# Optimization experiments

Hardware: AMD Instinct MI355X
Metric: run time of the kernel (lower is better)

## Reference

```python
import jax, jax.numpy as jnp
import numpy as np

N_ITEMS = 512
TABLE_SAMPLES = 2048
FULL_SIZE = 32768
PADDED_SIZE = 65536
BATCH = 8
N_EVENTS = 64


def setup_inputs() -> dict:
    key = jax.random.key(0)
    k1, k2, k3 = jax.random.split(key, 3)
    selections = jax.random.normal(k1, (BATCH, N_EVENTS, N_ITEMS), dtype=jnp.float32)
    # Envelopes init: uniform(-1,1) * linspace(1,0)**uniform(50,100) per item
    base = jax.random.uniform(k2, (N_ITEMS, TABLE_SAMPLES), minval=-1.0, maxval=1.0)
    exps = jax.random.uniform(jax.random.fold_in(k2, 1), (N_ITEMS, 1), minval=50.0, maxval=100.0)
    ramp = jnp.linspace(1.0, 0.0, TABLE_SAMPLES)[None, :]
    items = (base * ramp ** exps).astype(jnp.float32)
    # postprocess multiplies by uniform(-0.02, 0.02) noise of the interpolated shape
    noise = jax.random.uniform(k3, (BATCH, N_EVENTS, FULL_SIZE), minval=-0.02, maxval=0.02, dtype=jnp.float32)
    return {"selections": selections, "items": items, "noise": noise}


def reference(selections, items, noise):
    # preprocess_items: shift/scale into [0, ~1]
    items = items - items.min()
    items = items / (items.max() + 0.001)

    # select_items(..., type='sparse_softmax'): softmax over items, keep only
    # the max entry (scaled one-hot), then weighted combine against the table.
    sm = jax.nn.softmax(selections, axis=-1)                      # [b, e, n]
    w = jnp.max(sm, axis=-1, keepdims=True)                       # [b, e, 1]
    hard = jax.nn.one_hot(jnp.argmax(sm, axis=-1), sm.shape[-1], dtype=sm.dtype)
    sel = hard * w                                                # sparse one-hot weights
    selected = jnp.einsum('ben,nt->bet', sel, items)              # [b, e, T]

    # interpolate_last_axis: linear interpolation (half-pixel centers) to FULL_SIZE
    in_size = selected.shape[-1]
    pos = (jnp.arange(FULL_SIZE, dtype=jnp.float32) + 0.5) * (in_size / FULL_SIZE) - 0.5
    pos = jnp.clip(pos, 0.0, in_size - 1)
    lo = jnp.floor(pos).astype(jnp.int32)
    hi = jnp.minimum(lo + 1, in_size - 1)
    frac = (pos - lo).astype(selected.dtype)
    amp = selected[..., lo] * (1.0 - frac) + selected[..., hi] * frac  # [b, e, FULL]

    # multiply by noise, pad to PADDED_SIZE
    amp = amp * noise
    pad = jnp.zeros(amp.shape[:-1] + (PADDED_SIZE - FULL_SIZE,), dtype=amp.dtype)
    return jnp.concatenate([amp, pad], axis=-1)                   # [b, e, PADDED]
```

## Files before the change

kernel.cpp:

```cpp
#include <hip/hip_runtime.h>
#include <math.h>

constexpr int N_ITEMS = 512;
constexpr int TS      = 2048;
constexpr int FULL    = 32768;
constexpr int PADDED  = 65536;
constexpr int NPAIR   = 512;
constexpr int SPLIT   = 4;

using f4 = __attribute__((ext_vector_type(4))) float;

__device__ __forceinline__ unsigned fenc(float f) {
    unsigned u = __float_as_uint(f);
    return (u & 0x80000000u) ? ~u : (u | 0x80000000u);
}
__device__ __forceinline__ float fdec(unsigned e) {
    return __uint_as_float((e & 0x80000000u) ? (e & 0x7FFFFFFFu) : ~e);
}


__global__ void __launch_bounds__(256) k_prep(const f4* __restrict__ items4,
                                              const float* __restrict__ sel,
                                              unsigned* __restrict__ ws_min,
                                              unsigned* __restrict__ ws_max,
                                              int* __restrict__ ws_idx,
                                              float* __restrict__ ws_w) {
    __shared__ unsigned smin[4], smax[4];
    int blk = blockIdx.x;
    int tid = threadIdx.x;

    if (blk < 256) {
        unsigned lmin = 0xFFFFFFFFu, lmax = 0u;
        const int NV = (N_ITEMS * TS) / 4;
        for (int i = blk * 256 + tid; i < NV; i += 256 * 256) {
            f4 v = items4[i];
            unsigned e0 = fenc(v.x), e1 = fenc(v.y), e2 = fenc(v.z), e3 = fenc(v.w);
            lmin = min(min(min(lmin, e0), min(e1, e2)), e3);
            lmax = max(max(max(lmax, e0), max(e1, e2)), e3);
        }
        for (int off = 32; off > 0; off >>= 1) {
            lmin = min(lmin, (unsigned)__shfl_xor((int)lmin, off));
            lmax = max(lmax, (unsigned)__shfl_xor((int)lmax, off));
        }
        int wave = tid >> 6;
        if ((tid & 63) == 0) { smin[wave] = lmin; smax[wave] = lmax; }
        __syncthreads();
        if (tid == 0) {
            ws_min[blk] = min(min(smin[0], smin[1]), min(smin[2], smin[3]));
            ws_max[blk] = max(max(smax[0], smax[1]), max(smax[2], smax[3]));
        }
    } else {
        int p    = (blk - 256) * 4 + (tid >> 6);
        int lane = tid & 63;
        const float* s = sel + (size_t)p * N_ITEMS;
        float x[8];
        float vmax = -INFINITY;
        int   imax = 0x7FFFFFFF;
        #pragma unroll
        for (int k = 0; k < 8; ++k) {
            int i = lane + k * 64;
            x[k] = s[i];
            if (x[k] > vmax) { vmax = x[k]; imax = i; }
        }
        for (int off = 32; off > 0; off >>= 1) {
            float ov = __shfl_xor(vmax, off);
            int   oi = __shfl_xor(imax, off);
            if (ov > vmax || (ov == vmax && oi < imax)) { vmax = ov; imax = oi; }
        }
        float se = 0.0f;
        #pragma unroll
        for (int k = 0; k < 8; ++k) se += expf(x[k] - vmax);
        for (int off = 32; off > 0; off >>= 1) se += __shfl_xor(se, off);
        if (lane == 0) { ws_idx[p] = imax; ws_w[p] = 1.0f / se; }
    }
}

__global__ void __launch_bounds__(256, 8) k_main(const float* __restrict__ items,
                                                 const float* __restrict__ noise,
                                                 const unsigned* __restrict__ ws_min,
                                                 const unsigned* __restrict__ ws_max,
                                                 const int* __restrict__ ws_idx,
                                                 const float* __restrict__ ws_w,
                                                 float* __restrict__ out) {
    __shared__ float row[TS];

    int blk  = blockIdx.x;
    int p    = blk >> 2;
    int q    = blk & 3;
    int tid  = threadIdx.x;
    int lane = tid & 63;

    uint4 a = ((const uint4*)ws_min)[lane];
    uint4 c = ((const uint4*)ws_max)[lane];
    unsigned gmin = min(min(a.x, a.y), min(a.z, a.w));
    unsigned gmax = max(max(c.x, c.y), max(c.z, c.w));
    for (int off = 32; off > 0; off >>= 1) {
        gmin = min(gmin, (unsigned)__shfl_xor((int)gmin, off));
        gmax = max(gmax, (unsigned)__shfl_xor((int)gmax, off));
    }
    float minv  = fdec(gmin);
    float maxv  = fdec(gmax);
    float denom = (maxv - minv) + 0.001f;
    int   idx   = ws_idx[p];
    float scale = ws_w[p] / denom;
    float bias  = -minv * scale;

    constexpr int CHUNK  = FULL / SPLIT;
    constexpr int PCHUNK = (PADDED - FULL) / SPLIT;
    const f4* nz4  = (const f4*)(noise + (size_t)p * FULL + (size_t)q * CHUNK);
    f4*       o4   = (f4*)(out + (size_t)p * PADDED + (size_t)q * CHUNK);
    f4*       pad4 = (f4*)(out + (size_t)p * PADDED + FULL + (size_t)q * PCHUNK);
    int tbase = q * CHUNK;

    f4 nzv[8];
    #pragma unroll
    for (int k = 0; k < 8; ++k)
        nzv[k] = nz4[tid + k * 256];

    f4 z = {0.f, 0.f, 0.f, 0.f};
    #pragma unroll
    for (int k = 0; k < 8; ++k)
        pad4[tid + k * 256] = z;

    {
        const f4* it4 = (const f4*)(items + (size_t)idx * TS);
        f4 r0 = it4[tid];
        f4 r1 = it4[tid + 256];
        row[tid * 4 + 0] = fmaf(r0.x, scale, bias);
        row[tid * 4 + 1] = fmaf(r0.y, scale, bias);
        row[tid * 4 + 2] = fmaf(r0.z, scale, bias);
        row[tid * 4 + 3] = fmaf(r0.w, scale, bias);
        row[(tid + 256) * 4 + 0] = fmaf(r1.x, scale, bias);
        row[(tid + 256) * 4 + 1] = fmaf(r1.y, scale, bias);
        row[(tid + 256) * 4 + 2] = fmaf(r1.z, scale, bias);
        row[(tid + 256) * 4 + 3] = fmaf(r1.w, scale, bias);
    }
    __syncthreads();

    #pragma unroll
    for (int k = 0; k < 8; ++k) {
        int v  = tid + k * 256;
        int t0 = tbase + v * 4;
        float pos0 = ((float)t0 + 0.5f) * 0.0625f - 0.5f;
        f4 o;
        #pragma unroll
        for (int j = 0; j < 4; ++j) {
            float pj = fminf(fmaxf(pos0 + (float)j * 0.0625f, 0.0f), (float)(TS - 1));
            int   lj = (int)pj;
            int   hj = min(lj + 1, TS - 1);
            float fr = pj - (float)lj;
            float amp = row[lj] * (1.0f - fr) + row[hj] * fr;
            o[j] = amp * nzv[k][j];
        }
        o4[v] = o;
    }
}

extern "C" void kernel_launch(void* const* d_in, const int* in_sizes, int n_in,
                              void* d_out, int out_size, void* d_ws, size_t ws_size,
                              hipStream_t stream) {
    const float* sel   = (const float*)d_in[0];
    const float* items = (const float*)d_in[1];
    const float* noise = (const float*)d_in[2];
    float* out = (float*)d_out;

    unsigned* ws_min = (unsigned*)d_ws;
    unsigned* ws_max = (unsigned*)((char*)d_ws + 1024);
    int*      ws_idx = (int*)((char*)d_ws + 2048);
    float*    ws_w   = (float*)((char*)d_ws + 4096);

    hipLaunchKernelGGL(k_prep, dim3(384), dim3(256), 0, stream,
                       (const f4*)items, sel, ws_min, ws_max, ws_idx, ws_w);
    hipLaunchKernelGGL(k_main, dim3(NPAIR * SPLIT), dim3(256), 0, stream,
                       items, noise, ws_min, ws_max, ws_idx, ws_w, out);
}
```

Before: 39.62 us.

## Fuse prep and main kernels with atomic global min/max and spin-wait barrier

Merges the two-kernel pipeline into one launch. The first 256 blocks reduce the items min/max and publish the result through global atomics and a counter. Every block computes its own softmax argmax/weight, writes its padding and loads its rows, then spin-waits on the counter, with a timeout fallback that does a full local reduction. The affine normalization moves into the interpolation FMA and outputs use nontemporal stores. This removes one launch and the inter-kernel gap, but adds a memset launch, a cross-block spin dependency that relies on producer blocks being resident, and redundant per-block softmax work.

```diff
diff --git a/kernel.cpp b/kernel.cpp
--- a/kernel.cpp
+++ b/kernel.cpp
@@ -7,6 +7,8 @@
 constexpr int PADDED  = 65536;
 constexpr int NPAIR   = 512;
 constexpr int SPLIT   = 4;
+constexpr int NBLK    = NPAIR * SPLIT;
+constexpr int NPROD   = 256;
 
 using f4 = __attribute__((ext_vector_type(4))) float;
 
@@ -19,39 +21,48 @@
 }
 
 
-__global__ void __launch_bounds__(256) k_prep(const f4* __restrict__ items4,
-                                              const float* __restrict__ sel,
-                                              unsigned* __restrict__ ws_min,
-                                              unsigned* __restrict__ ws_max,
-                                              int* __restrict__ ws_idx,
-                                              float* __restrict__ ws_w) {
-    __shared__ unsigned smin[4], smax[4];
-    int blk = blockIdx.x;
-    int tid = threadIdx.x;
+__global__ void __launch_bounds__(256, 8) k_fused(const float* __restrict__ items,
+                                                  const float* __restrict__ sel,
+                                                  const float* __restrict__ noise,
+                                                  unsigned* __restrict__ ws,
+                                                  float* __restrict__ out) {
+    __shared__ float row[TS];
+    __shared__ unsigned sred[8];
+    __shared__ int s_idx;
+    __shared__ float s_w;
+    __shared__ int s_fb;
 
-    if (blk < 256) {
+    int b = blockIdx.x, t = threadIdx.x;
+    int lane = t & 63, wave = t >> 6;
+    int p = b >> 2, q = b & 3;
+
+    if (b < NPROD) {
+        const f4* it4 = (const f4*)items;
         unsigned lmin = 0xFFFFFFFFu, lmax = 0u;
-        const int NV = (N_ITEMS * TS) / 4;
-        for (int i = blk * 256 + tid; i < NV; i += 256 * 256) {
-            f4 v = items4[i];
+        #pragma unroll
+        for (int k = 0; k < 4; ++k) {
+            f4 v = it4[(size_t)k * 65536 + b * 256 + t];
             unsigned e0 = fenc(v.x), e1 = fenc(v.y), e2 = fenc(v.z), e3 = fenc(v.w);
-            lmin = min(min(min(lmin, e0), min(e1, e2)), e3);
-            lmax = max(max(max(lmax, e0), max(e1, e2)), e3);
+            lmin = min(lmin, min(min(e0, e1), min(e2, e3)));
+            lmax = max(lmax, max(max(e0, e1), max(e2, e3)));
         }
         for (int off = 32; off > 0; off >>= 1) {
             lmin = min(lmin, (unsigned)__shfl_xor((int)lmin, off));
             lmax = max(lmax, (unsigned)__shfl_xor((int)lmax, off));
         }
-        int wave = tid >> 6;
-        if ((tid & 63) == 0) { smin[wave] = lmin; smax[wave] = lmax; }
+        if (lane == 0) { sred[wave] = lmin; sred[4 + wave] = lmax; }
         __syncthreads();
-        if (tid == 0) {
-            ws_min[blk] = min(min(smin[0], smin[1]), min(smin[2], smin[3]));
-            ws_max[blk] = max(max(smax[0], smax[1]), max(smax[2], smax[3]));
+        if (t == 0) {
+            unsigned bmin = min(min(sred[0], sred[1]), min(sred[2], sred[3]));
+            unsigned bmax = max(max(sred[4], sred[5]), max(sred[6], sred[7]));
+            atomicMax(&ws[0], ~bmin);
+            atomicMax(&ws[1], bmax);
+            __threadfence();
+            atomicAdd(&ws[2], 1u);
         }
-    } else {
-        int p    = (blk - 256) * 4 + (tid >> 6);
-        int lane = tid & 63;
+    }
+
+    if (wave == 0) {
         const float* s = sel + (size_t)p * N_ITEMS;
         float x[8];
         float vmax = -INFINITY;
@@ -71,75 +82,82 @@
         #pragma unroll
         for (int k = 0; k < 8; ++k) se += expf(x[k] - vmax);
         for (int off = 32; off > 0; off >>= 1) se += __shfl_xor(se, off);
-        if (lane == 0) { ws_idx[p] = imax; ws_w[p] = 1.0f / se; }
+        if (lane == 0) { s_idx = imax; s_w = 1.0f / se; }
     }
-}
 
-__global__ void __launch_bounds__(256, 8) k_main(const float* __restrict__ items,
-                                                 const float* __restrict__ noise,
-                                                 const unsigned* __restrict__ ws_min,
-                                                 const unsigned* __restrict__ ws_max,
-                                                 const int* __restrict__ ws_idx,
-                                                 const float* __restrict__ ws_w,
-                                                 float* __restrict__ out) {
-    __shared__ float row[TS];
+    {
+        constexpr int PCHUNK = (PADDED - FULL) / SPLIT;
+        f4* pad4 = (f4*)(out + (size_t)p * PADDED + FULL + (size_t)q * PCHUNK);
+        f4 z = {0.f, 0.f, 0.f, 0.f};
+        #pragma unroll
+        for (int k = 0; k < 8; ++k)
+            __builtin_nontemporal_store(z, &pad4[t + k * 256]);
+    }
 
-    int blk  = blockIdx.x;
-    int p    = blk >> 2;
-    int q    = blk & 3;
-    int tid  = threadIdx.x;
-    int lane = tid & 63;
+    __syncthreads();
+    int   idx = s_idx;
+    float w   = s_w;
 
-    uint4 a = ((const uint4*)ws_min)[lane];
-    uint4 c = ((const uint4*)ws_max)[lane];
-    unsigned gmin = min(min(a.x, a.y), min(a.z, a.w));
-    unsigned gmax = max(max(c.x, c.y), max(c.z, c.w));
-    for (int off = 32; off > 0; off >>= 1) {
-        gmin = min(gmin, (unsigned)__shfl_xor((int)gmin, off));
-        gmax = max(gmax, (unsigned)__shfl_xor((int)gmax, off));
-    }
-    float minv  = fdec(gmin);
-    float maxv  = fdec(gmax);
-    float denom = (maxv - minv) + 0.001f;
-    int   idx   = ws_idx[p];
-    float scale = ws_w[p] / denom;
-    float bias  = -minv * scale;
+    const f4* it4 = (const f4*)(items + (size_t)idx * TS);
+    f4 r0 = it4[t];
+    f4 r1 = it4[t + 256];
 
-    constexpr int CHUNK  = FULL / SPLIT;
-    constexpr int PCHUNK = (PADDED - FULL) / SPLIT;
-    const f4* nz4  = (const f4*)(noise + (size_t)p * FULL + (size_t)q * CHUNK);
-    f4*       o4   = (f4*)(out + (size_t)p * PADDED + (size_t)q * CHUNK);
-    f4*       pad4 = (f4*)(out + (size_t)p * PADDED + FULL + (size_t)q * PCHUNK);
-    int tbase = q * CHUNK;
-
+    const f4* nz4 = (const f4*)(noise + (size_t)p * FULL + (size_t)q * (FULL / SPLIT));
     f4 nzv[8];
     #pragma unroll
     for (int k = 0; k < 8; ++k)
-        nzv[k] = nz4[tid + k * 256];
+        nzv[k] = nz4[t + k * 256];
 
-    f4 z = {0.f, 0.f, 0.f, 0.f};
-    #pragma unroll
-    for (int k = 0; k < 8; ++k)
-        pad4[tid + k * 256] = z;
+    ((f4*)row)[t]       = r0;
+    ((f4*)row)[t + 256] = r1;
 
-    {
-        const f4* it4 = (const f4*)(items + (size_t)idx * TS);
-        f4 r0 = it4[tid];
-        f4 r1 = it4[tid + 256];
-        row[tid * 4 + 0] = fmaf(r0.x, scale, bias);
-        row[tid * 4 + 1] = fmaf(r0.y, scale, bias);
-        row[tid * 4 + 2] = fmaf(r0.z, scale, bias);
-        row[tid * 4 + 3] = fmaf(r0.w, scale, bias);
-        row[(tid + 256) * 4 + 0] = fmaf(r1.x, scale, bias);
-        row[(tid + 256) * 4 + 1] = fmaf(r1.y, scale, bias);
-        row[(tid + 256) * 4 + 2] = fmaf(r1.z, scale, bias);
-        row[(tid + 256) * 4 + 3] = fmaf(r1.w, scale, bias);
+    if (t == 0) {
+        int fb = 0;
+        long long start = clock64();
+        while (__hip_atomic_load(&ws[2], __ATOMIC_ACQUIRE, __HIP_MEMORY_SCOPE_AGENT) < NPROD) {
+            __builtin_amdgcn_s_sleep(8);
+            if (clock64() - start > 10000000LL) { fb = 1; break; }
+        }
+        s_fb = fb;
     }
     __syncthreads();
 
+    float minv, maxv;
+    if (s_fb) {
+        const f4* a4 = (const f4*)items;
+        unsigned lmin = 0xFFFFFFFFu, lmax = 0u;
+        for (int i = t; i < (N_ITEMS * TS) / 4; i += 256) {
+            f4 v = a4[i];
+            unsigned e0 = fenc(v.x), e1 = fenc(v.y), e2 = fenc(v.z), e3 = fenc(v.w);
+            lmin = min(lmin, min(min(e0, e1), min(e2, e3)));
+            lmax = max(lmax, max(max(e0, e1), max(e2, e3)));
+        }
+        for (int off = 32; off > 0; off >>= 1) {
+            lmin = min(lmin, (unsigned)__shfl_xor((int)lmin, off));
+            lmax = max(lmax, (unsigned)__shfl_xor((int)lmax, off));
+        }
+        if (lane == 0) { sred[wave] = lmin; sred[4 + wave] = lmax; }
+        __syncthreads();
+        unsigned bmin = min(min(sred[0], sred[1]), min(sred[2], sred[3]));
+        unsigned bmax = max(max(sred[4], sred[5]), max(sred[6], sred[7]));
+        minv = fdec(bmin);
+        maxv = fdec(bmax);
+    } else {
+        unsigned im = __hip_atomic_load(&ws[0], __ATOMIC_RELAXED, __HIP_MEMORY_SCOPE_AGENT);
+        unsigned mx = __hip_atomic_load(&ws[1], __ATOMIC_RELAXED, __HIP_MEMORY_SCOPE_AGENT);
+        minv = fdec(~im);
+        maxv = fdec(mx);
+    }
+    float denom = (maxv - minv) + 0.001f;
+    float scale = w / denom;
+    float bias  = -minv * scale;
+
+    f4* o4 = (f4*)(out + (size_t)p * PADDED + (size_t)q * (FULL / SPLIT));
+    int tbase = q * (FULL / SPLIT);
+
     #pragma unroll
     for (int k = 0; k < 8; ++k) {
-        int v  = tid + k * 256;
+        int v  = t + k * 256;
         int t0 = tbase + v * 4;
         float pos0 = ((float)t0 + 0.5f) * 0.0625f - 0.5f;
         f4 o;
@@ -149,10 +167,10 @@
             int   lj = (int)pj;
             int   hj = min(lj + 1, TS - 1);
             float fr = pj - (float)lj;
-            float amp = row[lj] * (1.0f - fr) + row[hj] * fr;
-            o[j] = amp * nzv[k][j];
+            float raw = row[lj] * (1.0f - fr) + row[hj] * fr;
+            o[j] = fmaf(raw, scale, bias) * nzv[k][j];
         }
-        o4[v] = o;
+        __builtin_nontemporal_store(o, &o4[v]);
     }
 }
 
@@ -163,14 +181,9 @@
     const float* items = (const float*)d_in[1];
     const float* noise = (const float*)d_in[2];
     float* out = (float*)d_out;
+    unsigned* ws = (unsigned*)d_ws;
 
-    unsigned* ws_min = (unsigned*)d_ws;
-    unsigned* ws_max = (unsigned*)((char*)d_ws + 1024);
-    int*      ws_idx = (int*)((char*)d_ws + 2048);
-    float*    ws_w   = (float*)((char*)d_ws + 4096);
-
-    hipLaunchKernelGGL(k_prep, dim3(384), dim3(256), 0, stream,
-                       (const f4*)items, sel, ws_min, ws_max, ws_idx, ws_w);
-    hipLaunchKernelGGL(k_main, dim3(NPAIR * SPLIT), dim3(256), 0, stream,
-                       items, noise, ws_min, ws_max, ws_idx, ws_w, out);
+    hipMemsetAsync(ws, 0, 16, stream);
+    hipLaunchKernelGGL(k_fused, dim3(NBLK), dim3(256), 0, stream,
+                       items, sel, noise, ws, out);
 }
```

Measured after the change: 62.42 us. +57.5%, slower.
